# Optimization experiments

Hardware: AMD Instinct MI355X
Metric: run time of the kernel (lower is better)

Reference implementation:

```python
import jax, jax.numpy as jnp
import numpy as np

N = 100_000      # nodes
E = 1_600_000    # edges
IN = 256         # inchannel
H, D = 8, 16     # num_heads, out_feats per head (outchannel = 128)
SLOPE = 0.2      # DGL GATv2Conv default negative_slope


def setup_inputs() -> dict:
    key = jax.random.key(0)
    ks = jax.random.split(key, 8)
    s = 1.0 / np.sqrt(IN)
    return {
        "x": jax.random.normal(ks[0], (N, IN), jnp.float32),
        "src": jax.random.randint(ks[1], (E,), 0, N, jnp.int32),
        "dst": jax.random.randint(ks[2], (E,), 0, N, jnp.int32),
        "W_src": jax.random.uniform(ks[3], (IN, H * D), jnp.float32, -s, s),
        "b_src": jnp.zeros((H * D,), jnp.float32),
        "W_dst": jax.random.uniform(ks[4], (IN, H * D), jnp.float32, -s, s),
        "b_dst": jnp.zeros((H * D,), jnp.float32),
        "attn": jax.random.normal(ks[5], (H, D), jnp.float32) * 0.1,
        "W_res": jax.random.uniform(ks[6], (IN, H * D), jnp.float32, -s, s),
        "b_res": jnp.zeros((H * D,), jnp.float32),
    }


def reference(x, src, dst, W_src, b_src, W_dst, b_dst, attn, W_res, b_res):
    # GATv2: separate src/dst projections (share_weights=False)
    el = (x @ W_src + b_src).reshape(N, H, D)   # feat_src, (N,H,D)
    er = (x @ W_dst + b_dst).reshape(N, H, D)   # feat_dst, (N,H,D)

    # per-edge: e = LeakyReLU(el[u] + er[v]); score = sum(e * attn, -1)
    e = el[src] + er[dst]                        # (E,H,D)
    e = jnp.where(e > 0, e, SLOPE * e)           # LeakyReLU(0.2)
    score = jnp.einsum('ehd,hd->eh', e, attn)    # (E,H)

    # edge softmax over incoming edges of each destination node
    m = jax.ops.segment_max(score, dst, num_segments=N)   # (N,H)
    a = jnp.exp(score - m[dst])
    denom = jax.ops.segment_sum(a, dst, num_segments=N)   # (N,H)
    alpha = a / denom[dst]                                 # (E,H)

    # weighted aggregation of source features
    rst = jax.ops.segment_sum(alpha[:, :, None] * el[src], dst, num_segments=N)  # (N,H,D)

    # residual (in_feats != H*D -> linear res_fc)
    res = (x @ W_res + b_res).reshape(N, H, D)
    return (rst + res).reshape(N, H * D)
```

## Files before the change

kernel.cpp:

```cpp
#include <hip/hip_runtime.h>
#include <hip/hip_bf16.h>
#include <cstdint>

#define SLOPE 0.2f
#define IN_F 256
#define HD 128
#define BSH 8
#define BMAX 8192

typedef __attribute__((ext_vector_type(8))) short bf16x8;
typedef __attribute__((ext_vector_type(4))) float f32x4;

union BF8 { bf16x8 v; __hip_bfloat16 h[8]; };

__device__ inline float bf_lo(unsigned u) { unsigned w = u << 16; return __builtin_bit_cast(float, w); }
__device__ inline float bf_hi(unsigned u) { unsigned w = u & 0xffff0000u; return __builtin_bit_cast(float, w); }

__global__ void detect_kernel(const unsigned int* __restrict__ xw,
                              int* __restrict__ flag) {
    __shared__ int sh[256];
    int t = threadIdx.x;
    int cnt = 0;
    for (int i = t; i < 4096; i += 256) {
        unsigned e = (xw[i] >> 7) & 0xFF;
        cnt += (e >= 64u && e <= 191u) ? 1 : 0;
    }
    sh[t] = cnt;
    __syncthreads();
    for (int s = 128; s > 0; s >>= 1) {
        if (t < s) sh[t] += sh[t + s];
        __syncthreads();
    }
    if (t == 0) flag[0] = (sh[0] > 3300) ? 1 : 0;
}

__global__ void prep_kernel(const void* __restrict__ Ws, const void* __restrict__ Wd,
                            const void* __restrict__ Wr,
                            const void* __restrict__ bs, const void* __restrict__ bd,
                            const void* __restrict__ br,
                            const void* __restrict__ attn,
                            const int* __restrict__ flag,
                            __hip_bfloat16* __restrict__ Wp,
                            float* __restrict__ bfv, float* __restrict__ af) {
    int t = blockIdx.x * blockDim.x + threadIdx.x;
    int isb = flag[0];
    if (t < 3 * 8 * 8 * 64) {
        int lane = t & 63;
        int nt = (t >> 6) & 7;
        int kt = (t >> 9) & 7;
        int m  = t >> 12;
        const void* W = (m == 0) ? Ws : (m == 1) ? Wd : Wr;
        int n = nt * 16 + (lane & 15);
        int k0 = kt * 32 + (lane >> 4) * 8;
        size_t off = ((((size_t)m * 8 + kt) * 8 + nt) * 64 + lane) * 8;
#pragma unroll
        for (int j = 0; j < 8; j++) {
            size_t gi = (size_t)(k0 + j) * HD + n;
            Wp[off + j] = isb ? ((const __hip_bfloat16*)W)[gi]
                              : __float2bfloat16(((const float*)W)[gi]);
        }
    } else if (t < 3 * 8 * 8 * 64 + 384) {
        int j = t - 3 * 8 * 8 * 64;
        const void* b = (j < 128) ? bs : (j < 256 ? bd : br);
        int i = j & 127;
        bfv[j] = isb ? __bfloat162float(((const __hip_bfloat16*)b)[i])
                     : ((const float*)b)[i];
    } else if (t < 3 * 8 * 8 * 64 + 384 + 128) {
        int j = t - 3 * 8 * 8 * 64 - 384;
        af[j] = isb ? __bfloat162float(((const __hip_bfloat16*)attn)[j])
                    : ((const float*)attn)[j];
    }
}

template <bool ISB>
__device__ __forceinline__ void proj_body(
    const void* __restrict__ xv, const __hip_bfloat16* __restrict__ Wp,
    const float* __restrict__ bfv,
    __hip_bfloat16* __restrict__ el, __hip_bfloat16* __restrict__ er,
    __hip_bfloat16* __restrict__ resm,
    __hip_bfloat16* __restrict__ sxe, int Nn) {
    int tid = threadIdx.x;
    int lane = tid & 63;
    int nt = tid >> 6;
    int col = lane & 15;
    int quad = lane >> 4;
    int l7 = lane & 7;
    int r0 = blockIdx.x * 128;

#pragma unroll
    for (int i = 0; i < 8; i++) {
        int c = i * 512 + tid;
        int row = c >> 5;
        int unit = c & 31;
        int gr = r0 + row; if (gr >= Nn) gr = Nn - 1;
        BF8 tv;
        if (ISB) {
            tv.v = *(const bf16x8*)((const __hip_bfloat16*)xv + (size_t)gr * IN_F + (size_t)unit * 8);
        } else {
            const float* s = (const float*)xv + (size_t)gr * IN_F + (size_t)unit * 8;
            float4 p0 = *(const float4*)s;
            float4 p1 = *(const float4*)(s + 4);
            tv.h[0] = __float2bfloat16(p0.x); tv.h[1] = __float2bfloat16(p0.y);
            tv.h[2] = __float2bfloat16(p0.z); tv.h[3] = __float2bfloat16(p0.w);
            tv.h[4] = __float2bfloat16(p1.x); tv.h[5] = __float2bfloat16(p1.y);
            tv.h[6] = __float2bfloat16(p1.z); tv.h[7] = __float2bfloat16(p1.w);
        }
        int su = unit ^ ((row & 7) << 2);
        *(bf16x8*)(sxe + ((size_t)row * 32 + su) * 8) = tv.v;
    }

    bf16x8 wreg[3][8];
#pragma unroll
    for (int m = 0; m < 3; m++)
#pragma unroll
        for (int kt = 0; kt < 8; kt++)
            wreg[m][kt] = *(const bf16x8*)(
                Wp + ((((size_t)m * 8 + kt) * 8 + nt) * 64 + lane) * 8);

    __syncthreads();

    int swzu[8];
#pragma unroll
    for (int kt = 0; kt < 8; kt++) swzu[kt] = ((kt << 2) | quad) ^ (l7 << 2);

    const float bv0 = bfv[0 * HD + nt * 16 + col];
    const float bv1 = bfv[1 * HD + nt * 16 + col];
    const float bv2 = bfv[2 * HD + nt * 16 + col];

#pragma unroll 2
    for (int j = 0; j < 8; j++) {
        BF8 A[8];
#pragma unroll
        for (int kt = 0; kt < 8; kt++)
            A[kt].v = *(const bf16x8*)(
                sxe + ((size_t)j * 512 + (size_t)col * 32 + swzu[kt]) * 8);

        f32x4 a0 = (f32x4){0.f, 0.f, 0.f, 0.f};
        f32x4 a1 = (f32x4){0.f, 0.f, 0.f, 0.f};
        f32x4 a2 = (f32x4){0.f, 0.f, 0.f, 0.f};
#pragma unroll
        for (int kt = 0; kt < 8; kt++) {
            a0 = __builtin_amdgcn_mfma_f32_16x16x32_bf16(A[kt].v, wreg[0][kt], a0, 0, 0, 0);
            a1 = __builtin_amdgcn_mfma_f32_16x16x32_bf16(A[kt].v, wreg[1][kt], a1, 0, 0, 0);
            a2 = __builtin_amdgcn_mfma_f32_16x16x32_bf16(A[kt].v, wreg[2][kt], a2, 0, 0, 0);
        }

        int rbase = r0 + j * 16 + quad * 4;
#pragma unroll
        for (int r = 0; r < 4; r++) {
            int row = rbase + r;
            if (row < Nn) {
                size_t o = (size_t)row * HD + nt * 16 + col;
                el[o]   = __float2bfloat16(a0[r] + bv0);
                er[o]   = __float2bfloat16(a1[r] + bv1);
                resm[o] = __float2bfloat16(a2[r] + bv2);
            }
        }
    }
}

__global__ __launch_bounds__(512, 2) void proj_mfma_kernel(
    const void* __restrict__ xv, const __hip_bfloat16* __restrict__ Wp,
    const float* __restrict__ bfv, const int* __restrict__ flag,
    __hip_bfloat16* __restrict__ el, __hip_bfloat16* __restrict__ er,
    __hip_bfloat16* __restrict__ resm, int Nn) {
    __shared__ __hip_bfloat16 sxe[32768];
    if (flag[0]) proj_body<true>(xv, Wp, bfv, el, er, resm, sxe, Nn);
    else         proj_body<false>(xv, Wp, bfv, el, er, resm, sxe, Nn);
}

__global__ __launch_bounds__(256) void bhist_kernel(
    const int* __restrict__ dst, int* __restrict__ bcnt, int E, int NB) {
    __shared__ int cnt[512];
    int t = threadIdx.x;
    cnt[t] = 0; cnt[t + 256] = 0;
    __syncthreads();
    for (int i = blockIdx.x * 256 + t; i < E; i += gridDim.x * 256)
        atomicAdd(&cnt[dst[i] >> BSH], 1);
    __syncthreads();
    for (int j = t; j < NB; j += 256) {
        int c = cnt[j];
        if (c) atomicAdd(&bcnt[j], c);
    }
}

__global__ __launch_bounds__(512) void bscan_kernel(
    const int* __restrict__ bcnt, int* __restrict__ bbase,
    int* __restrict__ bcur, int NB) {
    __shared__ int sh[512];
    int t = threadIdx.x;
    sh[t] = (t < NB) ? bcnt[t] : 0;
    __syncthreads();
    for (int off = 1; off < 512; off <<= 1) {
        int x = sh[t];
        int y = (t >= off) ? sh[t - off] : 0;
        __syncthreads();
        sh[t] = x + y;
        __syncthreads();
    }
    if (t < NB) {
        int e = (t == 0) ? 0 : sh[t - 1];
        bbase[t] = e;
        bcur[t * 16] = e;
    }
}

__global__ void bin_kernel(const int* __restrict__ src, const int* __restrict__ dst,
                           int* __restrict__ bcur, unsigned* __restrict__ pairs, int E) {
    int t = blockIdx.x * blockDim.x + threadIdx.x;
    if (t < E) {
        int d = dst[t];
        int s = src[t];
        int b = d >> BSH;
        int pos = atomicAdd(&bcur[b * 16], 1);
        pairs[pos] = ((unsigned)(d & ((1 << BSH) - 1)) << 17) | (unsigned)s;
    }
}

__global__ __launch_bounds__(256) void scatter2_kernel(
    const unsigned* __restrict__ pairs, const int* __restrict__ bbase,
    const int* __restrict__ bcnt,
    int* __restrict__ deg, int* __restrict__ basep,
    int* __restrict__ srcs_sorted, int Nn) {
    __shared__ unsigned sp[BMAX];
    __shared__ int cnt[256];
    __shared__ int cur[256];
    int b = blockIdx.x;
    int t = threadIdx.x;
    int e0 = bbase[b];
    int ec = bcnt[b];
    bool fit = (ec <= BMAX);
    cnt[t] = 0;
    __syncthreads();
    for (int i = t; i < ec; i += 256) {
        unsigned p = pairs[e0 + i];
        if (fit) sp[i] = p;
        atomicAdd(&cnt[p >> 17], 1);
    }
    __syncthreads();
    int c = cnt[t];
    cur[t] = c;
    __syncthreads();
    for (int off = 1; off < 256; off <<= 1) {
        int x = cur[t];
        int y = (t >= off) ? cur[t - off] : 0;
        __syncthreads();
        cur[t] = x + y;
        __syncthreads();
    }
    int excl = cur[t] - c;
    int v = (b << BSH) + t;
    if (v < Nn) {
        deg[v] = c;
        basep[v] = e0 + excl;
    }
    __syncthreads();
    cur[t] = excl;
    __syncthreads();
    for (int i = t; i < ec; i += 256) {
        unsigned p = fit ? sp[i] : pairs[e0 + i];
        int hi = p >> 17;
        int lpos = atomicAdd(&cur[hi], 1);
        srcs_sorted[e0 + lpos] = (int)(p & 0x1FFFFu);
    }
}

__device__ __forceinline__ void agg_edge(unsigned u, float er0, float er1,
                                         float a0, float a1,
                                         float& l, float& acc0, float& acc1) {
    float x0 = bf_lo(u), x1 = bf_hi(u);
    float t0 = x0 + er0, t1 = x1 + er1;
    t0 = fmaxf(t0, SLOPE * t0); t1 = fmaxf(t1, SLOPE * t1);
    float p = t0 * a0 + t1 * a1;
    p += __shfl_xor(p, 1); p += __shfl_xor(p, 2); p += __shfl_xor(p, 4);
    float w = __expf(p);
    l += w; acc0 += w * x0; acc1 += w * x1;
}

__global__ __launch_bounds__(256) void node_agg_kernel(
    const unsigned* __restrict__ el32,
    const unsigned* __restrict__ er32,
    const unsigned* __restrict__ res32,
    const float* __restrict__ af,
    const int* __restrict__ base,
    const int* __restrict__ deg,
    const int* __restrict__ srcs_sorted,
    const int* __restrict__ flag,
    void* __restrict__ out,
    int Nn) {
    int wv = threadIdx.x >> 6;
    int lane = threadIdx.x & 63;
    int v = blockIdx.x * 4 + wv;
    if (v >= Nn) return;

    unsigned uer = er32[(size_t)v * 64 + lane];
    float er0 = bf_lo(uer), er1 = bf_hi(uer);
    float a0 = af[2 * lane], a1 = af[2 * lane + 1];
    int b0 = base[v];
    int dv = deg[v];

    float l = 0.f, acc0 = 0.f, acc1 = 0.f;
    for (int i0 = 0; i0 < dv; i0 += 64) {
        int chunk = dv - i0; if (chunk > 64) chunk = 64;
        int idx = (lane < chunk) ? srcs_sorted[b0 + i0 + lane] : 0;
        int i = 0;
        for (; i + 3 < chunk; i += 4) {
            int s0 = __shfl(idx, i);
            int s1 = __shfl(idx, i + 1);
            int s2 = __shfl(idx, i + 2);
            int s3 = __shfl(idx, i + 3);
            unsigned u0 = el32[(size_t)s0 * 64 + lane];
            unsigned u1 = el32[(size_t)s1 * 64 + lane];
            unsigned u2 = el32[(size_t)s2 * 64 + lane];
            unsigned u3 = el32[(size_t)s3 * 64 + lane];
            agg_edge(u0, er0, er1, a0, a1, l, acc0, acc1);
            agg_edge(u1, er0, er1, a0, a1, l, acc0, acc1);
            agg_edge(u2, er0, er1, a0, a1, l, acc0, acc1);
            agg_edge(u3, er0, er1, a0, a1, l, acc0, acc1);
        }
        for (; i < chunk; i++) {
            int s0 = __shfl(idx, i);
            unsigned u0 = el32[(size_t)s0 * 64 + lane];
            agg_edge(u0, er0, er1, a0, a1, l, acc0, acc1);
        }
    }

    float inv = (dv > 0 && l > 0.f) ? (1.f / l) : 0.f;
    unsigned ur = res32[(size_t)v * 64 + lane];
    float o0 = acc0 * inv + bf_lo(ur);
    float o1 = acc1 * inv + bf_hi(ur);
    if (flag[0]) {
        __hip_bfloat16 h0 = __float2bfloat16(o0);
        __hip_bfloat16 h1 = __float2bfloat16(o1);
        unsigned pk = (unsigned)__builtin_bit_cast(unsigned short, h0)
                    | ((unsigned)__builtin_bit_cast(unsigned short, h1) << 16);
        ((unsigned*)out)[(size_t)v * 64 + lane] = pk;
    } else {
        ((float2*)out)[(size_t)v * 64 + lane] = make_float2(o0, o1);
    }
}

extern "C" void kernel_launch(void* const* d_in, const int* in_sizes, int n_in,
                              void* d_out, int out_size, void* d_ws, size_t ws_size,
                              hipStream_t stream) {
    const void* x    = d_in[0];
    const int*  src  = (const int*)d_in[1];
    const int*  dst  = (const int*)d_in[2];
    const void* Ws   = d_in[3];
    const void* bs   = d_in[4];
    const void* Wd   = d_in[5];
    const void* bd   = d_in[6];
    const void* attn = d_in[7];
    const void* Wr   = d_in[8];
    const void* br   = d_in[9];

    const int Nn = in_sizes[0] / IN_F;
    const int E  = in_sizes[1];
    const int NB = (Nn + (1 << BSH) - 1) >> BSH;

    char* w = (char*)d_ws;
    auto take = [&](size_t bytes) {
        char* p = w;
        w += (bytes + 255) & ~(size_t)255;
        return p;
    };
    int*   flag = (int*)take(256);
    __hip_bfloat16* Wp = (__hip_bfloat16*)take((size_t)3 * 8 * 8 * 64 * 8 * 2);
    float* bfv  = (float*)take((size_t)384 * 4);
    float* af   = (float*)take((size_t)128 * 4);
    __hip_bfloat16* el   = (__hip_bfloat16*)take((size_t)Nn * HD * 2);
    __hip_bfloat16* er   = (__hip_bfloat16*)take((size_t)Nn * HD * 2);
    __hip_bfloat16* resm = (__hip_bfloat16*)take((size_t)Nn * HD * 2);
    int* deg     = (int*)take((size_t)Nn * 4);
    int* base    = (int*)take((size_t)Nn * 4);
    int* bcnt    = (int*)take((size_t)NB * 4);
    int* bbase   = (int*)take((size_t)NB * 4);
    int* bcur    = (int*)take((size_t)NB * 16 * 4);
    unsigned* pairs  = (unsigned*)take((size_t)E * 4);
    int* srcs_sorted = (int*)take((size_t)E * 4);

    hipMemsetAsync(bcnt, 0, (size_t)NB * 4, stream);

    detect_kernel<<<1, 256, 0, stream>>>((const unsigned int*)x, flag);

    prep_kernel<<<(3 * 8 * 8 * 64 + 512 + 255) / 256, 256, 0, stream>>>(
        Ws, Wd, Wr, bs, bd, br, attn, flag, Wp, bfv, af);

    proj_mfma_kernel<<<(Nn + 127) / 128, 512, 0, stream>>>(
        x, Wp, bfv, flag, el, er, resm, Nn);

    bhist_kernel<<<640, 256, 0, stream>>>(dst, bcnt, E, NB);
    bscan_kernel<<<1, 512, 0, stream>>>(bcnt, bbase, bcur, NB);
    bin_kernel<<<(E + 255) / 256, 256, 0, stream>>>(src, dst, bcur, pairs, E);
    scatter2_kernel<<<NB, 256, 0, stream>>>(pairs, bbase, bcnt, deg, base, srcs_sorted, Nn);

    node_agg_kernel<<<(Nn + 3) / 4, 256, 0, stream>>>(
        (const unsigned*)el, (const unsigned*)er, (const unsigned*)resm,
        af, base, deg, srcs_sorted, flag, d_out, Nn);
}
```

Measured before the change: 427.4 us.

## Aggregate bin-kernel atomics per block and unroll node aggregation by eight

After: 384.0 us. -10.1%, faster.

```diff
diff --git a/kernel.cpp b/kernel.cpp
--- a/kernel.cpp
+++ b/kernel.cpp
@@ -7,6 +7,7 @@
 #define HD 128
 #define BSH 8
 #define BMAX 8192
+#define EPB 8192
 
 typedef __attribute__((ext_vector_type(8))) short bf16x8;
 typedef __attribute__((ext_vector_type(4))) float f32x4;
@@ -205,15 +206,31 @@
     }
 }
 
-__global__ void bin_kernel(const int* __restrict__ src, const int* __restrict__ dst,
-                           int* __restrict__ bcur, unsigned* __restrict__ pairs, int E) {
-    int t = blockIdx.x * blockDim.x + threadIdx.x;
-    if (t < E) {
-        int d = dst[t];
-        int s = src[t];
+__global__ __launch_bounds__(256) void bin_kernel(
+    const int* __restrict__ src, const int* __restrict__ dst,
+    int* __restrict__ bcur, unsigned* __restrict__ pairs, int E, int NB) {
+    __shared__ int h[512];
+    __shared__ int cb[512];
+    int t = threadIdx.x;
+    h[t] = 0; h[t + 256] = 0;
+    __syncthreads();
+    int e0 = blockIdx.x * EPB;
+    int e1 = e0 + EPB; if (e1 > E) e1 = E;
+    for (int i = e0 + t; i < e1; i += 256)
+        atomicAdd(&h[dst[i] >> BSH], 1);
+    __syncthreads();
+    for (int b = t; b < NB; b += 256) {
+        int c = h[b];
+        cb[b] = c ? atomicAdd(&bcur[b * 16], c) : 0;
+        h[b] = 0;
+    }
+    __syncthreads();
+    for (int i = e0 + t; i < e1; i += 256) {
+        int d = dst[i];
+        int s = src[i];
         int b = d >> BSH;
-        int pos = atomicAdd(&bcur[b * 16], 1);
-        pairs[pos] = ((unsigned)(d & ((1 << BSH) - 1)) << 17) | (unsigned)s;
+        int lpos = atomicAdd(&h[b], 1);
+        pairs[cb[b] + lpos] = ((unsigned)(d & ((1 << BSH) - 1)) << 17) | (unsigned)s;
     }
 }
 
@@ -296,34 +313,49 @@
     unsigned uer = er32[(size_t)v * 64 + lane];
     float er0 = bf_lo(uer), er1 = bf_hi(uer);
     float a0 = af[2 * lane], a1 = af[2 * lane + 1];
-    int b0 = base[v];
-    int dv = deg[v];
-
-    float l = 0.f, acc0 = 0.f, acc1 = 0.f;
+    int b0 = __builtin_amdgcn_readfirstlane(base[v]);
+    int dv = __builtin_amdgcn_readfirstlane(deg[v]);
+
+    float la = 0.f, aa0 = 0.f, aa1 = 0.f;
+    float lb = 0.f, ab0 = 0.f, ab1 = 0.f;
     for (int i0 = 0; i0 < dv; i0 += 64) {
         int chunk = dv - i0; if (chunk > 64) chunk = 64;
         int idx = (lane < chunk) ? srcs_sorted[b0 + i0 + lane] : 0;
-        int i = 0;
-        for (; i + 3 < chunk; i += 4) {
-            int s0 = __shfl(idx, i);
-            int s1 = __shfl(idx, i + 1);
-            int s2 = __shfl(idx, i + 2);
-            int s3 = __shfl(idx, i + 3);
-            unsigned u0 = el32[(size_t)s0 * 64 + lane];
-            unsigned u1 = el32[(size_t)s1 * 64 + lane];
-            unsigned u2 = el32[(size_t)s2 * 64 + lane];
-            unsigned u3 = el32[(size_t)s3 * 64 + lane];
-            agg_edge(u0, er0, er1, a0, a1, l, acc0, acc1);
-            agg_edge(u1, er0, er1, a0, a1, l, acc0, acc1);
-            agg_edge(u2, er0, er1, a0, a1, l, acc0, acc1);
-            agg_edge(u3, er0, er1, a0, a1, l, acc0, acc1);
-        }
-        for (; i < chunk; i++) {
-            int s0 = __shfl(idx, i);
-            unsigned u0 = el32[(size_t)s0 * 64 + lane];
-            agg_edge(u0, er0, er1, a0, a1, l, acc0, acc1);
-        }
-    }
+        int ng = chunk >> 3;
+        for (int g = 0; g < ng; g++) {
+            int gb = g * 8;
+            int s0 = __builtin_amdgcn_readlane(idx, gb + 0);
+            int s1 = __builtin_amdgcn_readlane(idx, gb + 1);
+            int s2 = __builtin_amdgcn_readlane(idx, gb + 2);
+            int s3 = __builtin_amdgcn_readlane(idx, gb + 3);
+            int s4 = __builtin_amdgcn_readlane(idx, gb + 4);
+            int s5 = __builtin_amdgcn_readlane(idx, gb + 5);
+            int s6 = __builtin_amdgcn_readlane(idx, gb + 6);
+            int s7 = __builtin_amdgcn_readlane(idx, gb + 7);
+            unsigned u0 = el32[(size_t)(unsigned)s0 * 64 + lane];
+            unsigned u1 = el32[(size_t)(unsigned)s1 * 64 + lane];
+            unsigned u2 = el32[(size_t)(unsigned)s2 * 64 + lane];
+            unsigned u3 = el32[(size_t)(unsigned)s3 * 64 + lane];
+            unsigned u4 = el32[(size_t)(unsigned)s4 * 64 + lane];
+            unsigned u5 = el32[(size_t)(unsigned)s5 * 64 + lane];
+            unsigned u6 = el32[(size_t)(unsigned)s6 * 64 + lane];
+            unsigned u7 = el32[(size_t)(unsigned)s7 * 64 + lane];
+            agg_edge(u0, er0, er1, a0, a1, la, aa0, aa1);
+            agg_edge(u1, er0, er1, a0, a1, lb, ab0, ab1);
+            agg_edge(u2, er0, er1, a0, a1, la, aa0, aa1);
+            agg_edge(u3, er0, er1, a0, a1, lb, ab0, ab1);
+            agg_edge(u4, er0, er1, a0, a1, la, aa0, aa1);
+            agg_edge(u5, er0, er1, a0, a1, lb, ab0, ab1);
+            agg_edge(u6, er0, er1, a0, a1, la, aa0, aa1);
+            agg_edge(u7, er0, er1, a0, a1, lb, ab0, ab1);
+        }
+        for (int i = ng * 8; i < chunk; i++) {
+            int s0 = __builtin_amdgcn_readlane(idx, i);
+            unsigned u0 = el32[(size_t)(unsigned)s0 * 64 + lane];
+            agg_edge(u0, er0, er1, a0, a1, la, aa0, aa1);
+        }
+    }
+    float l = la + lb, acc0 = aa0 + ab0, acc1 = aa1 + ab1;
 
     float inv = (dv > 0 && l > 0.f) ? (1.f / l) : 0.f;
     unsigned ur = res32[(size_t)v * 64 + lane];
@@ -391,7 +423,7 @@
 
     bhist_kernel<<<640, 256, 0, stream>>>(dst, bcnt, E, NB);
     bscan_kernel<<<1, 512, 0, stream>>>(bcnt, bbase, bcur, NB);
-    bin_kernel<<<(E + 255) / 256, 256, 0, stream>>>(src, dst, bcur, pairs, E);
+    bin_kernel<<<(E + EPB - 1) / EPB, 256, 0, stream>>>(src, dst, bcur, pairs, E, NB);
     scatter2_kernel<<<NB, 256, 0, stream>>>(pairs, bbase, bcnt, deg, base, srcs_sorted, Nn);
 
     node_agg_kernel<<<(Nn + 3) / 4, 256, 0, stream>>>(
```
